# Kernel tuning notes

Hardware: AMD Instinct MI355X
Metric: run time of the kernel (lower is better)

The kernel has to match this reference:

```python
import jax, jax.numpy as jnp
import numpy as np

H, V, L = 1024, 50257, 512

def setup_inputs() -> dict:
    key = jax.random.key(0)
    ks = jax.random.split(key, 14)
    s = 0.02
    return {
        "input": jax.random.randint(ks[0], (1,), 0, V),
        "hidden": jax.random.normal(ks[1], (1, 1, H), jnp.float32),
        "encoder_outputs": jax.random.normal(ks[2], (L, H), jnp.float32),
        "emb": jax.random.normal(ks[3], (V, H), jnp.float32) * s,
        "attn_w": jax.random.normal(ks[4], (L, 2 * H), jnp.float32) * s,
        "attn_b": jnp.zeros((L,), jnp.float32),
        "comb_w": jax.random.normal(ks[5], (H, 2 * H), jnp.float32) * s,
        "comb_b": jnp.zeros((H,), jnp.float32),
        "w_ih": jax.random.normal(ks[6], (3 * H, H), jnp.float32) * s,
        "w_hh": jax.random.normal(ks[7], (3 * H, H), jnp.float32) * s,
        "b_ih": jnp.zeros((3 * H,), jnp.float32),
        "b_hh": jnp.zeros((3 * H,), jnp.float32),
        "out_w": jax.random.normal(ks[8], (V, H), jnp.float32) * s,
        "out_b": jnp.zeros((V,), jnp.float32),
    }

def reference(input, hidden, encoder_outputs, emb, attn_w, attn_b,
              comb_w, comb_b, w_ih, w_hh, b_ih, b_hh, out_w, out_b):
    # embedding lookup (dropout is identity in eval mode)
    e = emb[input]                       # (1, H)
    h0 = hidden[0]                       # (1, H)
    # attention over encoder outputs
    scores = jnp.concatenate([e, h0], axis=1) @ attn_w.T + attn_b   # (1, L)
    attn_weights = jax.nn.softmax(scores, axis=1)                    # (1, L)
    attn_applied = attn_weights @ encoder_outputs                    # (1, H)
    # combine + relu
    x = jnp.concatenate([e, attn_applied], axis=1) @ comb_w.T + comb_b
    x = jax.nn.relu(x)                   # (1, H)
    # single GRU step (PyTorch gate layout: r, z, n)
    gi = x @ w_ih.T + b_ih               # (1, 3H)
    gh = h0 @ w_hh.T + b_hh              # (1, 3H)
    i_r, i_z, i_n = jnp.split(gi, 3, axis=1)
    h_r, h_z, h_n = jnp.split(gh, 3, axis=1)
    r = jax.nn.sigmoid(i_r + h_r)
    z = jax.nn.sigmoid(i_z + h_z)
    n = jnp.tanh(i_n + r * h_n)
    h_new = (1.0 - z) * n + z * h0       # (1, H)
    # output projection + log_softmax
    logits = h_new @ out_w.T + out_b     # (1, V)
    out = jax.nn.log_softmax(logits, axis=1)
    return out, h_new[None], attn_weights
```

## Files before the change

### kernel.cpp

```cpp
#include <hip/hip_runtime.h>

#define H 1024
#define L 512
#define V 50257
#define LOGIT_BLOCKS 2048

__device__ __forceinline__ float dot4(float4 a, float4 b) {
    return a.x*b.x + a.y*b.y + a.z*b.z + a.w*b.w;
}

__device__ __forceinline__ float wave_reduce_sum(float v) {
    #pragma unroll
    for (int o = 32; o > 0; o >>= 1) v += __shfl_xor(v, o, 64);
    return v;
}

__global__ void k_pre(const float* __restrict__ emb, const int* __restrict__ input,
                      const float* __restrict__ hidden, const float* __restrict__ attn_w,
                      const float* __restrict__ attn_b, const float* __restrict__ w_hh,
                      const float* __restrict__ b_hh, const float* __restrict__ comb_w,
                      float* __restrict__ scores, float* __restrict__ gh, float* __restrict__ ce) {
    __shared__ float red[4];
    int task = blockIdx.x, t = threadIdx.x, lane = t & 63, wid = t >> 6;
    size_t erow = (size_t)input[0] * H;
    float acc;
    if (task < 512) {
        const float4* w = (const float4*)(attn_w + (size_t)task * (2 * H));
        acc = dot4(w[t], ((const float4*)(emb + erow))[t])
            + dot4(w[256 + t], ((const float4*)hidden)[t]);
    } else if (task < 3584) {
        int j = task - 512;
        acc = dot4(((const float4*)(w_hh + (size_t)j * H))[t], ((const float4*)hidden)[t]);
    } else {
        int h = task - 3584;
        acc = dot4(((const float4*)(comb_w + (size_t)h * (2 * H)))[t], ((const float4*)(emb + erow))[t]);
    }
    acc = wave_reduce_sum(acc);
    if (lane == 0) red[wid] = acc;
    __syncthreads();
    if (t == 0) {
        float s = red[0] + red[1] + red[2] + red[3];
        if (task < 512)       scores[task] = s + attn_b[task];
        else if (task < 3584) { int j = task - 512; gh[j] = s + b_hh[j]; }
        else                  ce[task - 3584] = s;
    }
}

__global__ void k_attn(const float* __restrict__ scores, const float* __restrict__ enc,
                       float* __restrict__ attn_out, float* __restrict__ attn_applied) {
    __shared__ float w[512];
    __shared__ float red[4];
    __shared__ float acc_lds[256];
    __shared__ float sM, sS;
    int t = threadIdx.x, lane = t & 63, wid = t >> 6;
    float s0 = scores[t], s1 = scores[t + 256];
    float m = fmaxf(s0, s1);
    #pragma unroll
    for (int o = 32; o > 0; o >>= 1) m = fmaxf(m, __shfl_xor(m, o, 64));
    if (lane == 0) red[wid] = m;
    __syncthreads();
    if (t == 0) sM = fmaxf(fmaxf(red[0], red[1]), fmaxf(red[2], red[3]));
    __syncthreads();
    float M = sM;
    float e0 = expf(s0 - M), e1 = expf(s1 - M);
    float s = wave_reduce_sum(e0 + e1);
    if (lane == 0) red[wid] = s;
    __syncthreads();
    if (t == 0) sS = red[0] + red[1] + red[2] + red[3];
    __syncthreads();
    float inv = 1.f / sS;
    w[t] = e0 * inv; w[t + 256] = e1 * inv;
    __syncthreads();
    if (blockIdx.x == 0) { attn_out[t] = w[t]; attn_out[t + 256] = w[t + 256]; }
    int col = blockIdx.x * 16 + (t & 15);
    int rc  = t >> 4;
    float acc = 0.f;
    #pragma unroll 8
    for (int l = rc; l < 512; l += 16) acc += w[l] * enc[(size_t)l * H + col];
    acc_lds[t] = acc;
    __syncthreads();
    #pragma unroll
    for (int st = 128; st >= 16; st >>= 1) {
        if (t < st) acc_lds[t] += acc_lds[t + st];
        __syncthreads();
    }
    if (t < 16) attn_applied[blockIdx.x * 16 + t] = acc_lds[t];
}

__global__ void k_combine2(const float* __restrict__ ce, const float* __restrict__ attn_applied,
                           const float* __restrict__ comb_w, const float* __restrict__ comb_b,
                           float* __restrict__ x) {
    __shared__ float red[4];
    int h = blockIdx.x, t = threadIdx.x, lane = t & 63, wid = t >> 6;
    float acc = dot4(((const float4*)(comb_w + (size_t)h * (2 * H) + H))[t],
                     ((const float4*)attn_applied)[t]);
    acc = wave_reduce_sum(acc);
    if (lane == 0) red[wid] = acc;
    __syncthreads();
    if (t == 0)
        x[h] = fmaxf(ce[h] + red[0] + red[1] + red[2] + red[3] + comb_b[h], 0.f);
}

__global__ void k_gru2(const float* __restrict__ w_ih, const float* __restrict__ b_ih,
                       const float* __restrict__ gh, const float* __restrict__ x,
                       const float* __restrict__ hidden, float* __restrict__ hnew) {
    __shared__ float red[12];
    int h = blockIdx.x, t = threadIdx.x, lane = t & 63, wid = t >> 6;
    float4 xv = ((const float4*)x)[t];
    float a0 = dot4(((const float4*)(w_ih + (size_t)h * H))[t], xv);
    float a1 = dot4(((const float4*)(w_ih + (size_t)(H + h) * H))[t], xv);
    float a2 = dot4(((const float4*)(w_ih + (size_t)(2 * H + h) * H))[t], xv);
    a0 = wave_reduce_sum(a0);
    a1 = wave_reduce_sum(a1);
    a2 = wave_reduce_sum(a2);
    if (lane == 0) { red[wid * 3] = a0; red[wid * 3 + 1] = a1; red[wid * 3 + 2] = a2; }
    __syncthreads();
    if (t == 0) {
        float g0 = 0.f, g1 = 0.f, g2 = 0.f;
        #pragma unroll
        for (int w2 = 0; w2 < 4; ++w2) {
            g0 += red[w2 * 3]; g1 += red[w2 * 3 + 1]; g2 += red[w2 * 3 + 2];
        }
        float r = 1.f / (1.f + expf(-(g0 + b_ih[h] + gh[h])));
        float z = 1.f / (1.f + expf(-(g1 + b_ih[H + h] + gh[H + h])));
        float n = tanhf(g2 + b_ih[2 * H + h] + r * gh[2 * H + h]);
        hnew[h] = (1.f - z) * n + z * hidden[h];
    }
}

__global__ void k_logits_lse(const float* __restrict__ out_w, const float* __restrict__ out_b,
                             const float* __restrict__ hvec, float* __restrict__ logits,
                             float* __restrict__ mpart, float* __restrict__ spart) {
    __shared__ float lm[4], ls[4];
    int lane = threadIdx.x & 63, wid = threadIdx.x >> 6;
    int gwave = blockIdx.x * 4 + wid;
    const int nwaves = LOGIT_BLOCKS * 4;
    float4 h4[4];
    #pragma unroll
    for (int j = 0; j < 4; ++j) h4[j] = ((const float4*)hvec)[j * 64 + lane];
    float m = -INFINITY, s = 0.f;
    for (int r = gwave; r < V; r += nwaves) {
        const float4* row = (const float4*)(out_w + (size_t)r * H);
        float acc = 0.f;
        #pragma unroll
        for (int j = 0; j < 4; ++j) acc += dot4(row[j * 64 + lane], h4[j]);
        acc = wave_reduce_sum(acc);
        float logit = acc + out_b[r];
        if (lane == 0) logits[r] = logit;
        if (logit > m) { s = s * expf(m - logit) + 1.f; m = logit; }
        else           { s += expf(logit - m); }
    }
    if (lane == 0) { lm[wid] = m; ls[wid] = s; }
    __syncthreads();
    if (threadIdx.x == 0) {
        float M = fmaxf(fmaxf(lm[0], lm[1]), fmaxf(lm[2], lm[3]));
        float S = 0.f;
        if (M > -INFINITY) {
            #pragma unroll
            for (int i = 0; i < 4; ++i) S += ls[i] * expf(lm[i] - M);
        }
        mpart[blockIdx.x] = M; spart[blockIdx.x] = S;
    }
}

__global__ void k_finalize(const float* __restrict__ mpart, const float* __restrict__ spart,
                           float* __restrict__ out) {
    __shared__ float lm[4], ls[4];
    __shared__ float sLogZ;
    int t = threadIdx.x, lane = t & 63, wid = t >> 6;
    float m = -INFINITY, s = 0.f;
    for (int i = t; i < LOGIT_BLOCKS; i += 256) {
        float m2 = mpart[i], s2 = spart[i];
        float mm = fmaxf(m, m2);
        if (mm > -INFINITY) s = s * expf(m - mm) + s2 * expf(m2 - mm);
        m = mm;
    }
    #pragma unroll
    for (int o = 32; o > 0; o >>= 1) {
        float m2 = __shfl_xor(m, o, 64), s2 = __shfl_xor(s, o, 64);
        float mm = fmaxf(m, m2);
        if (mm > -INFINITY) s = s * expf(m - mm) + s2 * expf(m2 - mm);
        m = mm;
    }
    if (lane == 0) { lm[wid] = m; ls[wid] = s; }
    __syncthreads();
    if (t == 0) {
        float M = fmaxf(fmaxf(lm[0], lm[1]), fmaxf(lm[2], lm[3]));
        float S = 0.f;
        #pragma unroll
        for (int i = 0; i < 4; ++i) S += ls[i] * expf(lm[i] - M);
        sLogZ = M + logf(S);
    }
    __syncthreads();
    int v = blockIdx.x * 256 + t;
    if (v < V) out[v] -= sLogZ;
}

extern "C" void kernel_launch(void* const* d_in, const int* in_sizes, int n_in,
                              void* d_out, int out_size, void* d_ws, size_t ws_size,
                              hipStream_t stream) {
    const int*   input  = (const int*)  d_in[0];
    const float* hidden = (const float*)d_in[1];
    const float* enc    = (const float*)d_in[2];
    const float* emb    = (const float*)d_in[3];
    const float* attn_w = (const float*)d_in[4];
    const float* attn_b = (const float*)d_in[5];
    const float* comb_w = (const float*)d_in[6];
    const float* comb_b = (const float*)d_in[7];
    const float* w_ih   = (const float*)d_in[8];
    const float* w_hh   = (const float*)d_in[9];
    const float* b_ih   = (const float*)d_in[10];
    const float* b_hh   = (const float*)d_in[11];
    const float* out_w  = (const float*)d_in[12];
    const float* out_b  = (const float*)d_in[13];

    float* out   = (float*)d_out;
    float* hnew  = out + V;
    float* attnw = out + V + H;

    float* ws           = (float*)d_ws;
    float* scores       = ws;
    float* gh           = ws + 512;
    float* ce           = ws + 3584;
    float* attn_applied = ws + 4608;
    float* xbuf         = ws + 5632;
    float* mpart        = ws + 6656;
    float* spart        = ws + 8704;

    k_pre        <<<4608, 256, 0, stream>>>(emb, input, hidden, attn_w, attn_b,
                                            w_hh, b_hh, comb_w, scores, gh, ce);
    k_attn       <<<64, 256, 0, stream>>>(scores, enc, attnw, attn_applied);
    k_combine2   <<<1024, 256, 0, stream>>>(ce, attn_applied, comb_w, comb_b, xbuf);
    k_gru2       <<<1024, 256, 0, stream>>>(w_ih, b_ih, gh, xbuf, hidden, hnew);
    k_logits_lse <<<LOGIT_BLOCKS, 256, 0, stream>>>(out_w, out_b, hnew, out, mpart, spart);
    k_finalize   <<<(V + 255) / 256, 256, 0, stream>>>(mpart, spart, out);
}
```

Before: 59.83 us.

## Fuse attention-apply with combine matvec via atomic partial sums

The attention-apply kernel now uses 128 blocks of 8 columns each. Each block multiplies its slice of attn_applied by the matching column slice of comb_w and atomically adds the partial sums into an x accumulator. This removes the separate combine kernel launch. The accumulator is zeroed by an extra block in the pre kernel, and the bias plus ReLU move into the GRU kernel. In exchange, 128 blocks issue atomic adds to 1024 floats, the accumulation order becomes nondeterministic, and comb_w is read with small strided float4 loads.

```diff
diff --git a/kernel.cpp b/kernel.cpp
--- a/kernel.cpp
+++ b/kernel.cpp
@@ -4,6 +4,8 @@
 #define L 512
 #define V 50257
 #define LOGIT_BLOCKS 2048
+#define ATTN_BLOCKS 128
+#define COLS 8
 
 __device__ __forceinline__ float dot4(float4 a, float4 b) {
     return a.x*b.x + a.y*b.y + a.z*b.z + a.w*b.w;
@@ -19,9 +21,15 @@
                       const float* __restrict__ hidden, const float* __restrict__ attn_w,
                       const float* __restrict__ attn_b, const float* __restrict__ w_hh,
                       const float* __restrict__ b_hh, const float* __restrict__ comb_w,
-                      float* __restrict__ scores, float* __restrict__ gh, float* __restrict__ ce) {
+                      const float* __restrict__ comb_b,
+                      float* __restrict__ scores, float* __restrict__ gh,
+                      float* __restrict__ ce, float* __restrict__ xacc) {
     __shared__ float red[4];
     int task = blockIdx.x, t = threadIdx.x, lane = t & 63, wid = t >> 6;
+    if (task == 4608) {
+        ((float4*)xacc)[t] = make_float4(0.f, 0.f, 0.f, 0.f);
+        return;
+    }
     size_t erow = (size_t)input[0] * H;
     float acc;
     if (task < 512) {
@@ -42,17 +50,18 @@
         float s = red[0] + red[1] + red[2] + red[3];
         if (task < 512)       scores[task] = s + attn_b[task];
         else if (task < 3584) { int j = task - 512; gh[j] = s + b_hh[j]; }
-        else                  ce[task - 3584] = s;
-    }
-}
-
-__global__ void k_attn(const float* __restrict__ scores, const float* __restrict__ enc,
-                       float* __restrict__ attn_out, float* __restrict__ attn_applied) {
+        else                  { int h = task - 3584; ce[h] = s + comb_b[h]; }
+    }
+}
+
+__global__ void k_attn_fused(const float* __restrict__ scores, const float* __restrict__ enc,
+                             const float* __restrict__ comb_w,
+                             float* __restrict__ attn_out, float* __restrict__ xacc) {
     __shared__ float w[512];
     __shared__ float red[4];
-    __shared__ float acc_lds[256];
+    __shared__ float s_acc[256];
     __shared__ float sM, sS;
-    int t = threadIdx.x, lane = t & 63, wid = t >> 6;
+    int t = threadIdx.x, lane = t & 63, wid = t >> 6, b = blockIdx.x;
     float s0 = scores[t], s1 = scores[t + 256];
     float m = fmaxf(s0, s1);
     #pragma unroll
@@ -63,50 +72,52 @@
     __syncthreads();
     float M = sM;
     float e0 = expf(s0 - M), e1 = expf(s1 - M);
-    float s = wave_reduce_sum(e0 + e1);
-    if (lane == 0) red[wid] = s;
+    float ssum = wave_reduce_sum(e0 + e1);
+    if (lane == 0) red[wid] = ssum;
     __syncthreads();
     if (t == 0) sS = red[0] + red[1] + red[2] + red[3];
     __syncthreads();
     float inv = 1.f / sS;
     w[t] = e0 * inv; w[t + 256] = e1 * inv;
     __syncthreads();
-    if (blockIdx.x == 0) { attn_out[t] = w[t]; attn_out[t + 256] = w[t + 256]; }
-    int col = blockIdx.x * 16 + (t & 15);
-    int rc  = t >> 4;
+    if (b == 0) { attn_out[t] = w[t]; attn_out[t + 256] = w[t + 256]; }
+    int col0 = b * COLS;
+    int c  = t & 7;
+    int rc = t >> 3;
     float acc = 0.f;
-    #pragma unroll 8
-    for (int l = rc; l < 512; l += 16) acc += w[l] * enc[(size_t)l * H + col];
-    acc_lds[t] = acc;
-    __syncthreads();
-    #pragma unroll
-    for (int st = 128; st >= 16; st >>= 1) {
-        if (t < st) acc_lds[t] += acc_lds[t + st];
+    #pragma unroll 4
+    for (int l = rc; l < 512; l += 32) acc += w[l] * enc[(size_t)l * H + col0 + c];
+    s_acc[t] = acc;
+    __syncthreads();
+    #pragma unroll
+    for (int st = 128; st >= 8; st >>= 1) {
+        if (t < st) s_acc[t] += s_acc[t + st];
         __syncthreads();
     }
-    if (t < 16) attn_applied[blockIdx.x * 16 + t] = acc_lds[t];
-}
-
-__global__ void k_combine2(const float* __restrict__ ce, const float* __restrict__ attn_applied,
-                           const float* __restrict__ comb_w, const float* __restrict__ comb_b,
-                           float* __restrict__ x) {
-    __shared__ float red[4];
-    int h = blockIdx.x, t = threadIdx.x, lane = t & 63, wid = t >> 6;
-    float acc = dot4(((const float4*)(comb_w + (size_t)h * (2 * H) + H))[t],
-                     ((const float4*)attn_applied)[t]);
-    acc = wave_reduce_sum(acc);
-    if (lane == 0) red[wid] = acc;
-    __syncthreads();
-    if (t == 0)
-        x[h] = fmaxf(ce[h] + red[0] + red[1] + red[2] + red[3] + comb_b[h], 0.f);
-}
-
-__global__ void k_gru2(const float* __restrict__ w_ih, const float* __restrict__ b_ih,
-                       const float* __restrict__ gh, const float* __restrict__ x,
-                       const float* __restrict__ hidden, float* __restrict__ hnew) {
+    float4 aa0 = make_float4(s_acc[0], s_acc[1], s_acc[2], s_acc[3]);
+    float4 aa1 = make_float4(s_acc[4], s_acc[5], s_acc[6], s_acc[7]);
+    #pragma unroll
+    for (int i = 0; i < 4; ++i) {
+        int h = t + 256 * i;
+        const float4* c2 = (const float4*)(comb_w + (size_t)h * (2 * H) + H + col0);
+        float p = dot4(c2[0], aa0) + dot4(c2[1], aa1);
+        atomicAdd(&xacc[h], p);
+    }
+}
+
+__global__ void k_gru3(const float* __restrict__ w_ih, const float* __restrict__ b_ih,
+                       const float* __restrict__ gh, const float* __restrict__ xacc,
+                       const float* __restrict__ ce, const float* __restrict__ hidden,
+                       float* __restrict__ hnew) {
     __shared__ float red[12];
     int h = blockIdx.x, t = threadIdx.x, lane = t & 63, wid = t >> 6;
-    float4 xv = ((const float4*)x)[t];
+    float4 xa = ((const float4*)xacc)[t];
+    float4 cv = ((const float4*)ce)[t];
+    float4 xv;
+    xv.x = fmaxf(xa.x + cv.x, 0.f);
+    xv.y = fmaxf(xa.y + cv.y, 0.f);
+    xv.z = fmaxf(xa.z + cv.z, 0.f);
+    xv.w = fmaxf(xa.w + cv.w, 0.f);
     float a0 = dot4(((const float4*)(w_ih + (size_t)h * H))[t], xv);
     float a1 = dot4(((const float4*)(w_ih + (size_t)(H + h) * H))[t], xv);
     float a2 = dot4(((const float4*)(w_ih + (size_t)(2 * H + h) * H))[t], xv);
@@ -218,20 +229,18 @@
     float* hnew  = out + V;
     float* attnw = out + V + H;
 
-    float* ws           = (float*)d_ws;
-    float* scores       = ws;
-    float* gh           = ws + 512;
-    float* ce           = ws + 3584;
-    float* attn_applied = ws + 4608;
-    float* xbuf         = ws + 5632;
-    float* mpart        = ws + 6656;
-    float* spart        = ws + 8704;
-
-    k_pre        <<<4608, 256, 0, stream>>>(emb, input, hidden, attn_w, attn_b,
-                                            w_hh, b_hh, comb_w, scores, gh, ce);
-    k_attn       <<<64, 256, 0, stream>>>(scores, enc, attnw, attn_applied);
-    k_combine2   <<<1024, 256, 0, stream>>>(ce, attn_applied, comb_w, comb_b, xbuf);
-    k_gru2       <<<1024, 256, 0, stream>>>(w_ih, b_ih, gh, xbuf, hidden, hnew);
+    float* ws     = (float*)d_ws;
+    float* scores = ws;
+    float* gh     = ws + 512;
+    float* ce     = ws + 3584;
+    float* xacc   = ws + 4608;
+    float* mpart  = ws + 5632;
+    float* spart  = ws + 7680;
+
+    k_pre        <<<4609, 256, 0, stream>>>(emb, input, hidden, attn_w, attn_b,
+                                            w_hh, b_hh, comb_w, comb_b, scores, gh, ce, xacc);
+    k_attn_fused <<<ATTN_BLOCKS, 256, 0, stream>>>(scores, enc, comb_w, attnw, xacc);
+    k_gru3       <<<1024, 256, 0, stream>>>(w_ih, b_ih, gh, xacc, ce, hidden, hnew);
     k_logits_lse <<<LOGIT_BLOCKS, 256, 0, stream>>>(out_w, out_b, hnew, out, mpart, spart);
     k_finalize   <<<(V + 255) / 256, 256, 0, stream>>>(mpart, spart, out);
 }
```

After: 63.19 us. 5.6% more time.
